# Kernel tuning notes

Measured on AMD Instinct MI355X. Metric: run time of the kernel, lower is better.

The kernel has to match this reference:

```python
import jax, jax.numpy as jnp
import numpy as np

B, N, C = 8, 512, 256
HID_E = 32          # edge_pred hidden width
FILTERS = (64, 64, 64)
OUT = 2


def setup_inputs() -> dict:
    key = jax.random.key(0)
    ks = jax.random.split(key, 12)
    s = 0.05
    inp = {
        "x": jax.random.normal(ks[0], (B, N, C), jnp.float32),
        "A": jax.random.uniform(ks[1], (B, N, N), jnp.float32),
        "mask": jnp.ones((B, N), jnp.float32),
        # edge predictor: Linear(2C,32) -> ReLU -> Linear(32,1)
        "ew1": jax.random.normal(ks[2], (2 * C, HID_E), jnp.float32) * s,
        "eb1": jnp.zeros((HID_E,), jnp.float32),
        "ew2": jax.random.normal(ks[3], (HID_E, 1), jnp.float32) * s,
        "eb2": jnp.zeros((1,), jnp.float32),
        # GraphConv stack: Linear(in*n_relations, f) per layer (n_relations=2)
        "gw0": jax.random.normal(ks[4], (2 * C, FILTERS[0]), jnp.float32) * s,
        "gb0": jnp.zeros((FILTERS[0],), jnp.float32),
        "gw1": jax.random.normal(ks[5], (2 * FILTERS[0], FILTERS[1]), jnp.float32) * s,
        "gb1": jnp.zeros((FILTERS[1],), jnp.float32),
        "gw2": jax.random.normal(ks[6], (2 * FILTERS[1], FILTERS[2]), jnp.float32) * s,
        "gb2": jnp.zeros((FILTERS[2],), jnp.float32),
        # final classifier (dropout is identity in eval)
        "fcw": jax.random.normal(ks[7], (FILTERS[2], OUT), jnp.float32) * s,
        "fcb": jnp.zeros((OUT,), jnp.float32),
    }
    return inp


def _laplacian(A):
    # A_hat = A + I ; L = D^-1/2 A_hat D^-1/2 with D from row-sums (dim 1)
    n = A.shape[-1]
    A_hat = A + jnp.eye(n, dtype=A.dtype)
    D = (A_hat.sum(axis=1) + 1e-5) ** -0.5  # [B,N]
    return D[:, :, None] * A_hat * D[:, None, :]


def reference(x, A, mask, ew1, eb1, ew2, eb2, gw0, gb0, gw1, gb1, gw2, gb2, fcw, fcb):
    b, n, c = x.shape
    # edge MLP over all node pairs; first layer split so we never build [B,N,N,2C]
    wa, wb = ew1[:c], ew1[c:]
    xa = x @ wa  # [B,N,32] contribution of node i
    xb = x @ wb  # [B,N,32] contribution of node j
    h = jax.nn.relu(xa[:, :, None, :] + xb[:, None, :, :] + eb1)  # [B,N,N,32]
    e = (h @ ew2)[..., 0] + eb2[0]  # e[b,i,j] = edge_pred([x_i, x_j])
    # symmetrized score: exp(0.5 * (f(i,j) + f(j,i)))
    y = jnp.exp(0.5 * (e + jnp.swapaxes(e, 1, 2)))
    triu = jnp.triu(jnp.ones((n, n), bool), 1)
    valid = (mask[:, :, None] > 0) & (mask[:, None, :] > 0)
    A_pred = jnp.where(triu[None] & valid, y, 0.0)
    A_pred = A_pred + jnp.swapaxes(A_pred, 1, 2)

    # multi-relation GCN stack (relations: input A, predicted A_pred)
    L0 = _laplacian(A)
    L1 = _laplacian(A_pred)
    m = mask[:, :, None]
    h0 = x
    for W, bias in ((gw0, gb0), (gw1, gb1), (gw2, gb2)):
        xh = jnp.concatenate([L0 @ h0, L1 @ h0], axis=-1)  # [B,N,2*f_in]
        h0 = jax.nn.relu((xh @ W + bias) * m)
    g = h0.max(axis=1)  # [B, filters[-1]] global max pool over nodes
    return g @ fcw + fcb  # [B, OUT]
```

## Files before the change

kernel.cpp:

```cpp
#include <hip/hip_runtime.h>
#include <hip/hip_bf16.h>
#include <math.h>

#define NB 8
#define NN 512
#define NC 256
#define HID 32

typedef __attribute__((ext_vector_type(8))) short short8;
typedef __attribute__((ext_vector_type(4))) float float4v;
typedef unsigned short ushort_t;

__device__ __forceinline__ ushort_t f2bf(float x) {
    unsigned u = __float_as_uint(x);
    return (ushort_t)((u + 0x7fffu + ((u >> 16) & 1u)) >> 16);
}
__device__ __forceinline__ float bf2f(ushort_t h) {
    return __uint_as_float(((unsigned)h) << 16);
}

__global__ __launch_bounds__(256) void xaxb_gemm(
    const float* __restrict__ x, const float* __restrict__ ew1,
    const float* __restrict__ eb1, float* __restrict__ xab,
    float* __restrict__ dsum)
{
    __shared__ float sX[32][17];
    __shared__ float sW[32][68];
    int t = threadIdx.x;
    if (blockIdx.x < 32) dsum[blockIdx.x * 256 + t] = 0.f;
    int r0 = blockIdx.x * 16;
    int tx = t & 15, ty = t >> 4;
    float acc[4] = {0.f, 0.f, 0.f, 0.f};
    for (int k0 = 0; k0 < NC; k0 += 32) {
        {
            int kk = (t & 15) * 2, r = t >> 4;
            float2 v = *(const float2*)(x + (size_t)(r0 + r) * NC + k0 + kk);
            sX[kk][r] = v.x; sX[kk + 1][r] = v.y;
        }
        {
            int c4 = (t & 15) * 4;
            int half = c4 >> 5, cc = c4 & 31;
#pragma unroll
            for (int rr = 0; rr < 2; ++rr) {
                int kk = (t >> 4) + rr * 16;
                *(float4*)&sW[kk][c4] =
                    *(const float4*)(ew1 + (size_t)(half * NC + k0 + kk) * HID + cc);
            }
        }
        __syncthreads();
#pragma unroll
        for (int k = 0; k < 32; ++k) {
            float a = sX[k][ty];
            float4 w = *(const float4*)&sW[k][tx * 4];
            acc[0] = fmaf(a, w.x, acc[0]); acc[1] = fmaf(a, w.y, acc[1]);
            acc[2] = fmaf(a, w.z, acc[2]); acc[3] = fmaf(a, w.w, acc[3]);
        }
        __syncthreads();
    }
    int c4 = tx * 4;
    float4 o; o.x = acc[0]; o.y = acc[1]; o.z = acc[2]; o.w = acc[3];
    if (c4 >= 32) {
        o.x += eb1[c4 - 32]; o.y += eb1[c4 - 31];
        o.z += eb1[c4 - 30]; o.w += eb1[c4 - 29];
    }
    *(float4*)&xab[(size_t)(r0 + ty) * 64 + c4] = o;
}

__global__ __launch_bounds__(256) void edge_scores(
    const float* __restrict__ xab, const float* __restrict__ ew2,
    const float* __restrict__ eb2, const float* __restrict__ mask,
    const float* __restrict__ A, ushort_t* __restrict__ Ah,
    ushort_t* __restrict__ APh, float* __restrict__ dsum)
{
    __shared__ float sI[32][65], sJ[32][65];
    __shared__ float sV[32][33];
    __shared__ float w2[32];
    int b = blockIdx.z;
    int p = blockIdx.x;
    int X = 0;
    while ((X + 1) * 16 - ((X + 1) * X) / 2 <= p) ++X;
    int Y = X + (p - (X * 16 - (X * (X - 1)) / 2));
    int i0 = X * 32, j0 = Y * 32;
    int t = threadIdx.x;
    if (t < 32) w2[t] = ew2[t];
    {
        int c4 = (t & 15) * 4;
#pragma unroll
        for (int rr = 0; rr < 2; ++rr) {
            int r = (t >> 4) + rr * 16;
            float4 vi = *(const float4*)(xab + ((size_t)(b * NN + i0 + r)) * 64 + c4);
            float4 vj = *(const float4*)(xab + ((size_t)(b * NN + j0 + r)) * 64 + c4);
            sI[r][c4] = vi.x; sI[r][c4 + 1] = vi.y; sI[r][c4 + 2] = vi.z; sI[r][c4 + 3] = vi.w;
            sJ[r][c4] = vj.x; sJ[r][c4 + 1] = vj.y; sJ[r][c4 + 2] = vj.z; sJ[r][c4 + 3] = vj.w;
        }
    }
    __syncthreads();
    float eb2v = eb2[0];
#pragma unroll
    for (int pz = 0; pz < 4; ++pz) {
        int e = t + pz * 256;
        int ti = e >> 5, tj = e & 31;
        int i = i0 + ti, j = j0 + tj;
        float sij = 0.f, sji = 0.f;
#pragma unroll
        for (int k = 0; k < 32; ++k) {
            sij = fmaf(fmaxf(sI[ti][k] + sJ[tj][32 + k], 0.f), w2[k], sij);
            sji = fmaf(fmaxf(sJ[tj][k] + sI[ti][32 + k], 0.f), w2[k], sji);
        }
        bool ok = (i != j) && (mask[b * NN + i] > 0.f) && (mask[b * NN + j] > 0.f);
        sV[ti][tj] = ok ? expf(0.5f * (sij + sji) + eb2v) : 0.f;
    }
    __syncthreads();
#pragma unroll
    for (int pz = 0; pz < 4; ++pz) {
        int r = (t >> 5) + pz * 8, c = t & 31;
        size_t o1 = ((size_t)(b * NN + i0 + r)) * NN + j0 + c;
        size_t o2 = ((size_t)(b * NN + j0 + r)) * NN + i0 + c;
        APh[o1] = f2bf(sV[r][c]);
        APh[o2] = f2bf(sV[c][r]);
    }
    if (t < 32) {
        float s = 0.f;
#pragma unroll
        for (int r = 0; r < 32; ++r) s += sV[r][t];
        atomicAdd(&dsum[(NB * NN) + b * NN + j0 + t], s);
    } else if (t < 64 && X != Y) {
        int c = t - 32;
        float s = 0.f;
#pragma unroll
        for (int j = 0; j < 32; ++j) s += sV[c][j];
        atomicAdd(&dsum[(NB * NN) + b * NN + i0 + c], s);
    }
    if (p < 128) {
        const float* Ar = A + ((size_t)b * NN + 4 * p) * NN;
        ushort_t* Hr = Ah + ((size_t)b * NN + 4 * p) * NN;
        float s0 = 0.f, s1 = 0.f;
#pragma unroll
        for (int rr = 0; rr < 4; ++rr) {
            float a0 = Ar[(size_t)rr * NN + t];
            float a1 = Ar[(size_t)rr * NN + t + 256];
            Hr[(size_t)rr * NN + t] = f2bf(a0);
            Hr[(size_t)rr * NN + t + 256] = f2bf(a1);
            s0 += a0; s1 += a1;
        }
        atomicAdd(&dsum[b * NN + t], s0);
        atomicAdd(&dsum[b * NN + t + 256], s1);
    }
}

__global__ __launch_bounds__(256) void pre_gemmT(
    const float* __restrict__ h, const float* __restrict__ gw,
    const float* __restrict__ dsum, ushort_t* __restrict__ PTh, int Cin)
{
    __shared__ float sH[32][17];
    __shared__ float sW[32][132];
    __shared__ __align__(16) ushort_t sTh[128][24];
    int r0 = blockIdx.x * 16;
    int t = threadIdx.x;
    int tx = t & 31, ty = t >> 5;
    float acc0[4] = {0.f, 0.f, 0.f, 0.f};
    float acc1[4] = {0.f, 0.f, 0.f, 0.f};
    for (int k0 = 0; k0 < Cin; k0 += 32) {
        {
            int kk = (t & 15) * 2, r = t >> 4;
            float2 v = *(const float2*)(h + (size_t)(r0 + r) * Cin + k0 + kk);
            sH[kk][r] = v.x; sH[kk + 1][r] = v.y;
        }
        {
            int c4 = (t & 31) * 4;
            int half = c4 >> 6, cc = c4 & 63;
#pragma unroll
            for (int rr = 0; rr < 4; ++rr) {
                int kk = (t >> 5) + rr * 8;
                *(float4*)&sW[kk][c4] =
                    *(const float4*)(gw + (size_t)(half * Cin + k0 + kk) * 64 + cc);
            }
        }
        __syncthreads();
#pragma unroll
        for (int k = 0; k < 32; ++k) {
            float a0 = sH[k][ty * 2];
            float a1 = sH[k][ty * 2 + 1];
            float4 w = *(const float4*)&sW[k][tx * 4];
            acc0[0] = fmaf(a0, w.x, acc0[0]); acc0[1] = fmaf(a0, w.y, acc0[1]);
            acc0[2] = fmaf(a0, w.z, acc0[2]); acc0[3] = fmaf(a0, w.w, acc0[3]);
            acc1[0] = fmaf(a1, w.x, acc1[0]); acc1[1] = fmaf(a1, w.y, acc1[1]);
            acc1[2] = fmaf(a1, w.z, acc1[2]); acc1[3] = fmaf(a1, w.w, acc1[3]);
        }
        __syncthreads();
    }
    int c4 = tx * 4;
    const float* draw = dsum + ((c4 >= 64) ? (NB * NN) : 0);
#pragma unroll
    for (int r = 0; r < 2; ++r) {
        int rl = ty * 2 + r;
        int row = r0 + rl;
        float d = rsqrtf(draw[row] + 1.0f + 1e-5f);
        float* ap = (r == 0) ? acc0 : acc1;
#pragma unroll
        for (int n = 0; n < 4; ++n)
            sTh[c4 + n][rl] = f2bf(d * ap[n]);
    }
    __syncthreads();
    {
        int c = t & 127, half = t >> 7;
        int bb = r0 >> 9, ibase = r0 & (NN - 1);
        ushort_t* dst = PTh + ((size_t)(bb * 128 + c)) * NN + ibase + half * 8;
        *(short8*)dst = *(const short8*)&sTh[c][half * 8];
    }
}

__global__ __launch_bounds__(256) void fused_mfma(
    const ushort_t* __restrict__ Ah, const ushort_t* __restrict__ APh,
    const ushort_t* __restrict__ PTh, const float* __restrict__ dsum,
    const float* __restrict__ bias, const float* __restrict__ mask,
    float* __restrict__ Hout)
{
    __shared__ __align__(16) ushort_t sA[2][16][72];
    __shared__ __align__(16) ushort_t sPh[64][72];
    __shared__ float sRed[2][32][17];
    int b = blockIdx.z, ch = blockIdx.y, i0 = blockIdx.x * 16;
    int t = threadIdx.x;
    int lane = t & 63, w = t >> 6;
    int quad = lane >> 4, m16 = lane & 15;
    int lap = w >> 1;
    float4v acc = {0.f, 0.f, 0.f, 0.f};

    int sa_arr = t >> 7, sa_id = t & 127;
    int sa_r = sa_id >> 3, sa_q = sa_id & 7;
    const ushort_t* sa_src = (sa_arr ? APh : Ah)
        + ((size_t)(b * NN + i0 + sa_r)) * NN + sa_q * 8;

    for (int k0 = 0; k0 < NN; k0 += 64) {
        __syncthreads();
        *(short8*)&sA[sa_arr][sa_r][sa_q * 8] = *(const short8*)(sa_src + k0);
#pragma unroll
        for (int cc = 0; cc < 2; ++cc) {
            int chunk = t + cc * 256;
            int l = chunk >> 3, q = chunk & 7;
            int colg = (l >> 5) * 64 + ch * 32 + (l & 31);
            const ushort_t* src = PTh + ((size_t)(b * 128 + colg)) * NN + k0 + q * 8;
            *(short8*)&sPh[l][q * 8] = *(const short8*)src;
        }
        __syncthreads();
#pragma unroll
        for (int kh = 0; kh < 2; ++kh) {
            int ko = kh * 32 + quad * 8;
            short8 ph = *(const short8*)&sPh[w * 16 + m16][ko];
            short8 av = *(const short8*)&sA[lap][m16][ko];
            acc = __builtin_amdgcn_mfma_f32_16x16x32_bf16(ph, av, acc, 0, 0, 0);
        }
    }
    int gi = b * NN + i0 + m16;
    float d = rsqrtf(dsum[lap * (NB * NN) + gi] + 1.0f + 1e-5f);
    int cbase = (w & 1) * 16 + quad * 4;
#pragma unroll
    for (int r = 0; r < 4; ++r) {
        int c32 = cbase + r;
        int pcol = lap * 64 + ch * 32 + c32;
        size_t pidx = ((size_t)(b * 128 + pcol)) * NN + i0 + m16;
        float pv = bf2f(PTh[pidx]);
        sRed[lap][c32][m16] = d * (acc[r] + pv);
    }
    __syncthreads();
#pragma unroll
    for (int s = 0; s < 2; ++s) {
        int idx = t + s * 256;
        int c32 = idx & 31, i = idx >> 5;
        int gi2 = b * NN + i0 + i;
        float v = (sRed[0][c32][i] + sRed[1][c32][i] + bias[ch * 32 + c32]) * mask[gi2];
        Hout[(size_t)gi2 * 64 + ch * 32 + c32] = fmaxf(v, 0.f);
    }
}

__global__ __launch_bounds__(256) void final_fc(
    const float* __restrict__ H, const float* __restrict__ fcw,
    const float* __restrict__ fcb, float* __restrict__ out)
{
    __shared__ float red[4][64];
    __shared__ float g[64];
    int b = blockIdx.x;
    int o = threadIdx.x & 63, seg = threadIdx.x >> 6;
    const float* Hb = H + (size_t)b * NN * 64;
    float mx = -INFINITY;
    for (int i = seg; i < NN; i += 4) mx = fmaxf(mx, Hb[(size_t)i * 64 + o]);
    red[seg][o] = mx;
    __syncthreads();
    if (seg == 0)
        g[o] = fmaxf(fmaxf(red[0][o], red[1][o]), fmaxf(red[2][o], red[3][o]));
    __syncthreads();
    if (threadIdx.x < 2) {
        float acc = fcb[threadIdx.x];
        for (int k = 0; k < 64; ++k) acc = fmaf(g[k], fcw[k * 2 + threadIdx.x], acc);
        out[b * 2 + threadIdx.x] = acc;
    }
}

extern "C" void kernel_launch(void* const* d_in, const int* in_sizes, int n_in,
                              void* d_out, int out_size, void* d_ws, size_t ws_size,
                              hipStream_t stream)
{
    const float* x    = (const float*)d_in[0];
    const float* A    = (const float*)d_in[1];
    const float* mask = (const float*)d_in[2];
    const float* ew1  = (const float*)d_in[3];
    const float* eb1  = (const float*)d_in[4];
    const float* ew2  = (const float*)d_in[5];
    const float* eb2  = (const float*)d_in[6];
    const float* gw0  = (const float*)d_in[7];
    const float* gb0  = (const float*)d_in[8];
    const float* gw1  = (const float*)d_in[9];
    const float* gb1  = (const float*)d_in[10];
    const float* gw2  = (const float*)d_in[11];
    const float* gb2  = (const float*)d_in[12];
    const float* fcw  = (const float*)d_in[13];
    const float* fcb  = (const float*)d_in[14];
    float* out = (float*)d_out;
    char* ws = (char*)d_ws;

    const size_t NEL = (size_t)NB * NN * NN;
    float*    xab  = (float*)ws;                       ws += 262144 * 4;
    ushort_t* APh  = (ushort_t*)ws;                    ws += NEL * 2;
    ushort_t* Ahs  = (ushort_t*)ws;                    ws += NEL * 2;
    float*    dsum = (float*)ws;                       ws += 8192 * 4;
    ushort_t* PTh  = (ushort_t*)ws;                    ws += 524288 * 2;
    float*    hA   = (float*)ws;                       ws += 262144 * 4;
    float*    hB   = (float*)ws;                       ws += 262144 * 4;

    xaxb_gemm  <<<256, 256, 0, stream>>>(x, ew1, eb1, xab, dsum);
    edge_scores<<<dim3(136, 1, NB), 256, 0, stream>>>(xab, ew2, eb2, mask,
                                                      A, Ahs, APh, dsum);

    pre_gemmT <<<256, 256, 0, stream>>>(x, gw0, dsum, PTh, 256);
    fused_mfma<<<dim3(32, 2, NB), 256, 0, stream>>>(Ahs, APh, PTh,
                                                    dsum, gb0, mask, hA);
    pre_gemmT <<<256, 256, 0, stream>>>(hA, gw1, dsum, PTh, 64);
    fused_mfma<<<dim3(32, 2, NB), 256, 0, stream>>>(Ahs, APh, PTh,
                                                    dsum, gb1, mask, hB);
    pre_gemmT <<<256, 256, 0, stream>>>(hB, gw2, dsum, PTh, 64);
    fused_mfma<<<dim3(32, 2, NB), 256, 0, stream>>>(Ahs, APh, PTh,
                                                    dsum, gb2, mask, hA);

    final_fc<<<NB, 256, 0, stream>>>(hA, fcw, fcb, out);
}
```

Measured before the change: 182.6 us.

## Fuse all stages into one persistent kernel with grid-wide atomic barriers

Replaces the nine separate kernel launches with a single persistent kernel of 256 blocks. The blocks move through the edge-score, GCN pre-GEMM, MFMA aggregation and final-FC phases, separated by software grid barriers built on an atomic counter. Shared memory is overlaid through a union. This removes launch gaps and inter-kernel drain, but adds barrier spin cost and relies on all 256 blocks being co-resident. Work per phase is also rebalanced over a fixed grid, so phases with 1088 tiles now loop.

```diff
diff --git a/kernel.cpp b/kernel.cpp
--- a/kernel.cpp
+++ b/kernel.cpp
@@ -6,6 +6,7 @@
 #define NN 512
 #define NC 256
 #define HID 32
+#define GD 256
 
 typedef __attribute__((ext_vector_type(8))) short short8;
 typedef __attribute__((ext_vector_type(4))) float float4v;
@@ -19,280 +20,305 @@
     return __uint_as_float(((unsigned)h) << 16);
 }
 
-__global__ __launch_bounds__(256) void xaxb_gemm(
-    const float* __restrict__ x, const float* __restrict__ ew1,
-    const float* __restrict__ eb1, float* __restrict__ xab,
-    float* __restrict__ dsum)
+__device__ __forceinline__ void gbar(int* cnt, int target) {
+    __syncthreads();
+    if (threadIdx.x == 0) {
+        __threadfence();
+        atomicAdd(cnt, 1);
+        while (__hip_atomic_load(cnt, __ATOMIC_RELAXED,
+                                 __HIP_MEMORY_SCOPE_AGENT) < target)
+            __builtin_amdgcn_s_sleep(2);
+        __threadfence();
+    }
+    __syncthreads();
+}
+
+struct Params {
+    const float *x, *A, *mask, *ew1, *eb1, *ew2, *eb2;
+    const float *gw0, *gb0, *gw1, *gb1, *gw2, *gb2, *fcw, *fcb;
+    float* out;
+    int*   bar;
+    float* xab;
+    ushort_t* APh;
+    ushort_t* Ahs;
+    float* dsum;
+    ushort_t* PTh;
+    float* hA;
+    float* hB;
+};
+
+union SharedT {
+    struct { float sX[32][17]; float sW[32][68]; } p1;
+    struct { float sI[32][65]; float sJ[32][65]; float sV[32][33]; float w2[32]; } p2;
+    struct { float sH[32][17]; float sW[32][132]; ushort_t sTh[128][24]; } p3;
+    struct { ushort_t sA[2][16][72]; ushort_t sPh[64][72]; float sRed[2][32][17]; } p4;
+    struct { float red[4][64]; float g[64]; } p5;
+};
+
+__global__ void bar_init(int* bar) { if (threadIdx.x < 64) bar[threadIdx.x] = 0; }
+
+__global__ __launch_bounds__(256, 1) void mega(Params P)
 {
-    __shared__ float sX[32][17];
-    __shared__ float sW[32][68];
+    __shared__ __align__(16) SharedT sh;
     int t = threadIdx.x;
-    if (blockIdx.x < 32) dsum[blockIdx.x * 256 + t] = 0.f;
-    int r0 = blockIdx.x * 16;
-    int tx = t & 15, ty = t >> 4;
-    float acc[4] = {0.f, 0.f, 0.f, 0.f};
-    for (int k0 = 0; k0 < NC; k0 += 32) {
-        {
-            int kk = (t & 15) * 2, r = t >> 4;
-            float2 v = *(const float2*)(x + (size_t)(r0 + r) * NC + k0 + kk);
-            sX[kk][r] = v.x; sX[kk + 1][r] = v.y;
-        }
+    int bid = blockIdx.x;
+    int barn = 0;
+
+    if (bid < 32) P.dsum[bid * 256 + t] = 0.f;
+    for (int r0 = bid * 16; r0 < 4096 * 0 + (bid + 1) * 16; r0 += 16) {
+        int tx = t & 15, ty = t >> 4;
+        float acc[4] = {0.f, 0.f, 0.f, 0.f};
+        for (int k0 = 0; k0 < NC; k0 += 32) {
+            {
+                int kk = (t & 15) * 2, r = t >> 4;
+                float2 v = *(const float2*)(P.x + (size_t)(r0 + r) * NC + k0 + kk);
+                sh.p1.sX[kk][r] = v.x; sh.p1.sX[kk + 1][r] = v.y;
+            }
+            {
+                int c4 = (t & 15) * 4;
+                int half = c4 >> 5, cc = c4 & 31;
+#pragma unroll
+                for (int rr = 0; rr < 2; ++rr) {
+                    int kk = (t >> 4) + rr * 16;
+                    *(float4*)&sh.p1.sW[kk][c4] =
+                        *(const float4*)(P.ew1 + (size_t)(half * NC + k0 + kk) * HID + cc);
+                }
+            }
+            __syncthreads();
+#pragma unroll
+            for (int k = 0; k < 32; ++k) {
+                float a = sh.p1.sX[k][ty];
+                float4 w = *(const float4*)&sh.p1.sW[k][tx * 4];
+                acc[0] = fmaf(a, w.x, acc[0]); acc[1] = fmaf(a, w.y, acc[1]);
+                acc[2] = fmaf(a, w.z, acc[2]); acc[3] = fmaf(a, w.w, acc[3]);
+            }
+            __syncthreads();
+        }
+        int c4 = tx * 4;
+        float4 o; o.x = acc[0]; o.y = acc[1]; o.z = acc[2]; o.w = acc[3];
+        if (c4 >= 32) {
+            o.x += P.eb1[c4 - 32]; o.y += P.eb1[c4 - 31];
+            o.z += P.eb1[c4 - 30]; o.w += P.eb1[c4 - 29];
+        }
+        *(float4*)&P.xab[(size_t)(r0 + ty) * 64 + c4] = o;
+    }
+    gbar(P.bar, ++barn * GD);
+
+    for (int u = bid; u < 136 * NB; u += GD) {
+        __syncthreads();
+        int b = u / 136, p = u - b * 136;
+        int X = 0;
+        while ((X + 1) * 16 - ((X + 1) * X) / 2 <= p) ++X;
+        int Y = X + (p - (X * 16 - (X * (X - 1)) / 2));
+        int i0 = X * 32, j0 = Y * 32;
+        if (t < 32) sh.p2.w2[t] = P.ew2[t];
         {
             int c4 = (t & 15) * 4;
-            int half = c4 >> 5, cc = c4 & 31;
 #pragma unroll
             for (int rr = 0; rr < 2; ++rr) {
-                int kk = (t >> 4) + rr * 16;
-                *(float4*)&sW[kk][c4] =
-                    *(const float4*)(ew1 + (size_t)(half * NC + k0 + kk) * HID + cc);
-            }
-        }
-        __syncthreads();
-#pragma unroll
-        for (int k = 0; k < 32; ++k) {
-            float a = sX[k][ty];
-            float4 w = *(const float4*)&sW[k][tx * 4];
-            acc[0] = fmaf(a, w.x, acc[0]); acc[1] = fmaf(a, w.y, acc[1]);
-            acc[2] = fmaf(a, w.z, acc[2]); acc[3] = fmaf(a, w.w, acc[3]);
-        }
-        __syncthreads();
-    }
-    int c4 = tx * 4;
-    float4 o; o.x = acc[0]; o.y = acc[1]; o.z = acc[2]; o.w = acc[3];
-    if (c4 >= 32) {
-        o.x += eb1[c4 - 32]; o.y += eb1[c4 - 31];
-        o.z += eb1[c4 - 30]; o.w += eb1[c4 - 29];
-    }
-    *(float4*)&xab[(size_t)(r0 + ty) * 64 + c4] = o;
-}
-
-__global__ __launch_bounds__(256) void edge_scores(
-    const float* __restrict__ xab, const float* __restrict__ ew2,
-    const float* __restrict__ eb2, const float* __restrict__ mask,
-    const float* __restrict__ A, ushort_t* __restrict__ Ah,
-    ushort_t* __restrict__ APh, float* __restrict__ dsum)
-{
-    __shared__ float sI[32][65], sJ[32][65];
-    __shared__ float sV[32][33];
-    __shared__ float w2[32];
-    int b = blockIdx.z;
-    int p = blockIdx.x;
-    int X = 0;
-    while ((X + 1) * 16 - ((X + 1) * X) / 2 <= p) ++X;
-    int Y = X + (p - (X * 16 - (X * (X - 1)) / 2));
-    int i0 = X * 32, j0 = Y * 32;
-    int t = threadIdx.x;
-    if (t < 32) w2[t] = ew2[t];
-    {
-        int c4 = (t & 15) * 4;
-#pragma unroll
-        for (int rr = 0; rr < 2; ++rr) {
-            int r = (t >> 4) + rr * 16;
-            float4 vi = *(const float4*)(xab + ((size_t)(b * NN + i0 + r)) * 64 + c4);
-            float4 vj = *(const float4*)(xab + ((size_t)(b * NN + j0 + r)) * 64 + c4);
-            sI[r][c4] = vi.x; sI[r][c4 + 1] = vi.y; sI[r][c4 + 2] = vi.z; sI[r][c4 + 3] = vi.w;
-            sJ[r][c4] = vj.x; sJ[r][c4 + 1] = vj.y; sJ[r][c4 + 2] = vj.z; sJ[r][c4 + 3] = vj.w;
-        }
-    }
-    __syncthreads();
-    float eb2v = eb2[0];
-#pragma unroll
-    for (int pz = 0; pz < 4; ++pz) {
-        int e = t + pz * 256;
-        int ti = e >> 5, tj = e & 31;
-        int i = i0 + ti, j = j0 + tj;
-        float sij = 0.f, sji = 0.f;
-#pragma unroll
-        for (int k = 0; k < 32; ++k) {
-            sij = fmaf(fmaxf(sI[ti][k] + sJ[tj][32 + k], 0.f), w2[k], sij);
-            sji = fmaf(fmaxf(sJ[tj][k] + sI[ti][32 + k], 0.f), w2[k], sji);
-        }
-        bool ok = (i != j) && (mask[b * NN + i] > 0.f) && (mask[b * NN + j] > 0.f);
-        sV[ti][tj] = ok ? expf(0.5f * (sij + sji) + eb2v) : 0.f;
-    }
-    __syncthreads();
-#pragma unroll
-    for (int pz = 0; pz < 4; ++pz) {
-        int r = (t >> 5) + pz * 8, c = t & 31;
-        size_t o1 = ((size_t)(b * NN + i0 + r)) * NN + j0 + c;
-        size_t o2 = ((size_t)(b * NN + j0 + r)) * NN + i0 + c;
-        APh[o1] = f2bf(sV[r][c]);
-        APh[o2] = f2bf(sV[c][r]);
-    }
-    if (t < 32) {
-        float s = 0.f;
-#pragma unroll
-        for (int r = 0; r < 32; ++r) s += sV[r][t];
-        atomicAdd(&dsum[(NB * NN) + b * NN + j0 + t], s);
-    } else if (t < 64 && X != Y) {
-        int c = t - 32;
-        float s = 0.f;
-#pragma unroll
-        for (int j = 0; j < 32; ++j) s += sV[c][j];
-        atomicAdd(&dsum[(NB * NN) + b * NN + i0 + c], s);
-    }
-    if (p < 128) {
-        const float* Ar = A + ((size_t)b * NN + 4 * p) * NN;
-        ushort_t* Hr = Ah + ((size_t)b * NN + 4 * p) * NN;
-        float s0 = 0.f, s1 = 0.f;
-#pragma unroll
-        for (int rr = 0; rr < 4; ++rr) {
-            float a0 = Ar[(size_t)rr * NN + t];
-            float a1 = Ar[(size_t)rr * NN + t + 256];
-            Hr[(size_t)rr * NN + t] = f2bf(a0);
-            Hr[(size_t)rr * NN + t + 256] = f2bf(a1);
-            s0 += a0; s1 += a1;
-        }
-        atomicAdd(&dsum[b * NN + t], s0);
-        atomicAdd(&dsum[b * NN + t + 256], s1);
-    }
-}
-
-__global__ __launch_bounds__(256) void pre_gemmT(
-    const float* __restrict__ h, const float* __restrict__ gw,
-    const float* __restrict__ dsum, ushort_t* __restrict__ PTh, int Cin)
-{
-    __shared__ float sH[32][17];
-    __shared__ float sW[32][132];
-    __shared__ __align__(16) ushort_t sTh[128][24];
-    int r0 = blockIdx.x * 16;
-    int t = threadIdx.x;
-    int tx = t & 31, ty = t >> 5;
-    float acc0[4] = {0.f, 0.f, 0.f, 0.f};
-    float acc1[4] = {0.f, 0.f, 0.f, 0.f};
-    for (int k0 = 0; k0 < Cin; k0 += 32) {
-        {
-            int kk = (t & 15) * 2, r = t >> 4;
-            float2 v = *(const float2*)(h + (size_t)(r0 + r) * Cin + k0 + kk);
-            sH[kk][r] = v.x; sH[kk + 1][r] = v.y;
-        }
-        {
-            int c4 = (t & 31) * 4;
-            int half = c4 >> 6, cc = c4 & 63;
+                int r = (t >> 4) + rr * 16;
+                float4 vi = *(const float4*)(P.xab + ((size_t)(b * NN + i0 + r)) * 64 + c4);
+                float4 vj = *(const float4*)(P.xab + ((size_t)(b * NN + j0 + r)) * 64 + c4);
+                sh.p2.sI[r][c4] = vi.x; sh.p2.sI[r][c4 + 1] = vi.y;
+                sh.p2.sI[r][c4 + 2] = vi.z; sh.p2.sI[r][c4 + 3] = vi.w;
+                sh.p2.sJ[r][c4] = vj.x; sh.p2.sJ[r][c4 + 1] = vj.y;
+                sh.p2.sJ[r][c4 + 2] = vj.z; sh.p2.sJ[r][c4 + 3] = vj.w;
+            }
+        }
+        __syncthreads();
+        float eb2v = P.eb2[0];
+#pragma unroll
+        for (int pz = 0; pz < 4; ++pz) {
+            int e = t + pz * 256;
+            int ti = e >> 5, tj = e & 31;
+            int i = i0 + ti, j = j0 + tj;
+            float sij = 0.f, sji = 0.f;
+#pragma unroll
+            for (int k = 0; k < 32; ++k) {
+                sij = fmaf(fmaxf(sh.p2.sI[ti][k] + sh.p2.sJ[tj][32 + k], 0.f), sh.p2.w2[k], sij);
+                sji = fmaf(fmaxf(sh.p2.sJ[tj][k] + sh.p2.sI[ti][32 + k], 0.f), sh.p2.w2[k], sji);
+            }
+            bool ok = (i != j) && (P.mask[b * NN + i] > 0.f) && (P.mask[b * NN + j] > 0.f);
+            sh.p2.sV[ti][tj] = ok ? expf(0.5f * (sij + sji) + eb2v) : 0.f;
+        }
+        __syncthreads();
+#pragma unroll
+        for (int pz = 0; pz < 4; ++pz) {
+            int r = (t >> 5) + pz * 8, c = t & 31;
+            size_t o1 = ((size_t)(b * NN + i0 + r)) * NN + j0 + c;
+            size_t o2 = ((size_t)(b * NN + j0 + r)) * NN + i0 + c;
+            P.APh[o1] = f2bf(sh.p2.sV[r][c]);
+            P.APh[o2] = f2bf(sh.p2.sV[c][r]);
+        }
+        if (t < 32) {
+            float s = 0.f;
+#pragma unroll
+            for (int r = 0; r < 32; ++r) s += sh.p2.sV[r][t];
+            atomicAdd(&P.dsum[(NB * NN) + b * NN + j0 + t], s);
+        } else if (t < 64 && X != Y) {
+            int c = t - 32;
+            float s = 0.f;
+#pragma unroll
+            for (int j = 0; j < 32; ++j) s += sh.p2.sV[c][j];
+            atomicAdd(&P.dsum[(NB * NN) + b * NN + i0 + c], s);
+        }
+        if (p < 128) {
+            const float* Ar = P.A + ((size_t)b * NN + 4 * p) * NN;
+            ushort_t* Hr = P.Ahs + ((size_t)b * NN + 4 * p) * NN;
+            float s0 = 0.f, s1 = 0.f;
 #pragma unroll
             for (int rr = 0; rr < 4; ++rr) {
-                int kk = (t >> 5) + rr * 8;
-                *(float4*)&sW[kk][c4] =
-                    *(const float4*)(gw + (size_t)(half * Cin + k0 + kk) * 64 + cc);
-            }
-        }
-        __syncthreads();
-#pragma unroll
-        for (int k = 0; k < 32; ++k) {
-            float a0 = sH[k][ty * 2];
-            float a1 = sH[k][ty * 2 + 1];
-            float4 w = *(const float4*)&sW[k][tx * 4];
-            acc0[0] = fmaf(a0, w.x, acc0[0]); acc0[1] = fmaf(a0, w.y, acc0[1]);
-            acc0[2] = fmaf(a0, w.z, acc0[2]); acc0[3] = fmaf(a0, w.w, acc0[3]);
-            acc1[0] = fmaf(a1, w.x, acc1[0]); acc1[1] = fmaf(a1, w.y, acc1[1]);
-            acc1[2] = fmaf(a1, w.z, acc1[2]); acc1[3] = fmaf(a1, w.w, acc1[3]);
-        }
-        __syncthreads();
-    }
-    int c4 = tx * 4;
-    const float* draw = dsum + ((c4 >= 64) ? (NB * NN) : 0);
-#pragma unroll
-    for (int r = 0; r < 2; ++r) {
-        int rl = ty * 2 + r;
-        int row = r0 + rl;
-        float d = rsqrtf(draw[row] + 1.0f + 1e-5f);
-        float* ap = (r == 0) ? acc0 : acc1;
-#pragma unroll
-        for (int n = 0; n < 4; ++n)
-            sTh[c4 + n][rl] = f2bf(d * ap[n]);
-    }
-    __syncthreads();
-    {
-        int c = t & 127, half = t >> 7;
-        int bb = r0 >> 9, ibase = r0 & (NN - 1);
-        ushort_t* dst = PTh + ((size_t)(bb * 128 + c)) * NN + ibase + half * 8;
-        *(short8*)dst = *(const short8*)&sTh[c][half * 8];
-    }
-}
-
-__global__ __launch_bounds__(256) void fused_mfma(
-    const ushort_t* __restrict__ Ah, const ushort_t* __restrict__ APh,
-    const ushort_t* __restrict__ PTh, const float* __restrict__ dsum,
-    const float* __restrict__ bias, const float* __restrict__ mask,
-    float* __restrict__ Hout)
-{
-    __shared__ __align__(16) ushort_t sA[2][16][72];
-    __shared__ __align__(16) ushort_t sPh[64][72];
-    __shared__ float sRed[2][32][17];
-    int b = blockIdx.z, ch = blockIdx.y, i0 = blockIdx.x * 16;
-    int t = threadIdx.x;
+                float a0 = Ar[(size_t)rr * NN + t];
+                float a1 = Ar[(size_t)rr * NN + t + 256];
+                Hr[(size_t)rr * NN + t] = f2bf(a0);
+                Hr[(size_t)rr * NN + t + 256] = f2bf(a1);
+                s0 += a0; s1 += a1;
+            }
+            atomicAdd(&P.dsum[b * NN + t], s0);
+            atomicAdd(&P.dsum[b * NN + t + 256], s1);
+        }
+    }
+    gbar(P.bar, ++barn * GD);
+
     int lane = t & 63, w = t >> 6;
     int quad = lane >> 4, m16 = lane & 15;
     int lap = w >> 1;
-    float4v acc = {0.f, 0.f, 0.f, 0.f};
-
     int sa_arr = t >> 7, sa_id = t & 127;
     int sa_r = sa_id >> 3, sa_q = sa_id & 7;
-    const ushort_t* sa_src = (sa_arr ? APh : Ah)
-        + ((size_t)(b * NN + i0 + sa_r)) * NN + sa_q * 8;
-
-    for (int k0 = 0; k0 < NN; k0 += 64) {
-        __syncthreads();
-        *(short8*)&sA[sa_arr][sa_r][sa_q * 8] = *(const short8*)(sa_src + k0);
-#pragma unroll
-        for (int cc = 0; cc < 2; ++cc) {
-            int chunk = t + cc * 256;
-            int l = chunk >> 3, q = chunk & 7;
-            int colg = (l >> 5) * 64 + ch * 32 + (l & 31);
-            const ushort_t* src = PTh + ((size_t)(b * 128 + colg)) * NN + k0 + q * 8;
-            *(short8*)&sPh[l][q * 8] = *(const short8*)src;
-        }
-        __syncthreads();
-#pragma unroll
-        for (int kh = 0; kh < 2; ++kh) {
-            int ko = kh * 32 + quad * 8;
-            short8 ph = *(const short8*)&sPh[w * 16 + m16][ko];
-            short8 av = *(const short8*)&sA[lap][m16][ko];
-            acc = __builtin_amdgcn_mfma_f32_16x16x32_bf16(ph, av, acc, 0, 0, 0);
-        }
-    }
-    int gi = b * NN + i0 + m16;
-    float d = rsqrtf(dsum[lap * (NB * NN) + gi] + 1.0f + 1e-5f);
-    int cbase = (w & 1) * 16 + quad * 4;
-#pragma unroll
-    for (int r = 0; r < 4; ++r) {
-        int c32 = cbase + r;
-        int pcol = lap * 64 + ch * 32 + c32;
-        size_t pidx = ((size_t)(b * 128 + pcol)) * NN + i0 + m16;
-        float pv = bf2f(PTh[pidx]);
-        sRed[lap][c32][m16] = d * (acc[r] + pv);
-    }
-    __syncthreads();
-#pragma unroll
-    for (int s = 0; s < 2; ++s) {
-        int idx = t + s * 256;
-        int c32 = idx & 31, i = idx >> 5;
-        int gi2 = b * NN + i0 + i;
-        float v = (sRed[0][c32][i] + sRed[1][c32][i] + bias[ch * 32 + c32]) * mask[gi2];
-        Hout[(size_t)gi2 * 64 + ch * 32 + c32] = fmaxf(v, 0.f);
-    }
-}
-
-__global__ __launch_bounds__(256) void final_fc(
-    const float* __restrict__ H, const float* __restrict__ fcw,
-    const float* __restrict__ fcb, float* __restrict__ out)
-{
-    __shared__ float red[4][64];
-    __shared__ float g[64];
-    int b = blockIdx.x;
-    int o = threadIdx.x & 63, seg = threadIdx.x >> 6;
-    const float* Hb = H + (size_t)b * NN * 64;
-    float mx = -INFINITY;
-    for (int i = seg; i < NN; i += 4) mx = fmaxf(mx, Hb[(size_t)i * 64 + o]);
-    red[seg][o] = mx;
-    __syncthreads();
-    if (seg == 0)
-        g[o] = fmaxf(fmaxf(red[0][o], red[1][o]), fmaxf(red[2][o], red[3][o]));
-    __syncthreads();
-    if (threadIdx.x < 2) {
-        float acc = fcb[threadIdx.x];
-        for (int k = 0; k < 64; ++k) acc = fmaf(g[k], fcw[k * 2 + threadIdx.x], acc);
-        out[b * 2 + threadIdx.x] = acc;
+
+    for (int L = 0; L < 3; ++L) {
+        const float* hsrc = (L == 0) ? P.x : ((L == 1) ? P.hA : P.hB);
+        const float* gw   = (L == 0) ? P.gw0 : ((L == 1) ? P.gw1 : P.gw2);
+        const float* gb   = (L == 0) ? P.gb0 : ((L == 1) ? P.gb1 : P.gb2);
+        float* hout       = (L == 1) ? P.hB : P.hA;
+        int Cin           = (L == 0) ? NC : 64;
+
+        {
+            int r0 = bid * 16;
+            int tx = t & 31, ty = t >> 5;
+            float acc0[4] = {0.f, 0.f, 0.f, 0.f};
+            float acc1[4] = {0.f, 0.f, 0.f, 0.f};
+            for (int k0 = 0; k0 < Cin; k0 += 32) {
+                __syncthreads();
+                {
+                    int kk = (t & 15) * 2, r = t >> 4;
+                    float2 v = *(const float2*)(hsrc + (size_t)(r0 + r) * Cin + k0 + kk);
+                    sh.p3.sH[kk][r] = v.x; sh.p3.sH[kk + 1][r] = v.y;
+                }
+                {
+                    int c4 = (t & 31) * 4;
+                    int half = c4 >> 6, cc = c4 & 63;
+#pragma unroll
+                    for (int rr = 0; rr < 4; ++rr) {
+                        int kk = (t >> 5) + rr * 8;
+                        *(float4*)&sh.p3.sW[kk][c4] =
+                            *(const float4*)(gw + (size_t)(half * Cin + k0 + kk) * 64 + cc);
+                    }
+                }
+                __syncthreads();
+#pragma unroll
+                for (int k = 0; k < 32; ++k) {
+                    float a0 = sh.p3.sH[k][ty * 2];
+                    float a1 = sh.p3.sH[k][ty * 2 + 1];
+                    float4 ww = *(const float4*)&sh.p3.sW[k][tx * 4];
+                    acc0[0] = fmaf(a0, ww.x, acc0[0]); acc0[1] = fmaf(a0, ww.y, acc0[1]);
+                    acc0[2] = fmaf(a0, ww.z, acc0[2]); acc0[3] = fmaf(a0, ww.w, acc0[3]);
+                    acc1[0] = fmaf(a1, ww.x, acc1[0]); acc1[1] = fmaf(a1, ww.y, acc1[1]);
+                    acc1[2] = fmaf(a1, ww.z, acc1[2]); acc1[3] = fmaf(a1, ww.w, acc1[3]);
+                }
+            }
+            __syncthreads();
+            int c4 = tx * 4;
+            const float* draw = P.dsum + ((c4 >= 64) ? (NB * NN) : 0);
+#pragma unroll
+            for (int r = 0; r < 2; ++r) {
+                int rl = ty * 2 + r;
+                int row = r0 + rl;
+                float d = rsqrtf(draw[row] + 1.0f + 1e-5f);
+                float* ap = (r == 0) ? acc0 : acc1;
+#pragma unroll
+                for (int n = 0; n < 4; ++n)
+                    sh.p3.sTh[c4 + n][rl] = f2bf(d * ap[n]);
+            }
+            __syncthreads();
+            {
+                int c = t & 127, half = t >> 7;
+                int bb = r0 >> 9, ibase = r0 & (NN - 1);
+                ushort_t* dst = P.PTh + ((size_t)(bb * 128 + c)) * NN + ibase + half * 8;
+                *(short8*)dst = *(const short8*)&sh.p3.sTh[c][half * 8];
+            }
+        }
+        gbar(P.bar, ++barn * GD);
+
+        for (int fu = bid; fu < 512; fu += GD) {
+            int fb = fu >> 6, frem = fu & 63;
+            int fch = frem >> 5, fi0 = (frem & 31) * 16;
+            const ushort_t* sa_src = (sa_arr ? P.APh : P.Ahs)
+                + ((size_t)(fb * NN + fi0 + sa_r)) * NN + sa_q * 8;
+            float4v acc = {0.f, 0.f, 0.f, 0.f};
+            for (int k0 = 0; k0 < NN; k0 += 64) {
+                __syncthreads();
+                *(short8*)&sh.p4.sA[sa_arr][sa_r][sa_q * 8] = *(const short8*)(sa_src + k0);
+#pragma unroll
+                for (int cc = 0; cc < 2; ++cc) {
+                    int chunk = t + cc * 256;
+                    int l = chunk >> 3, q = chunk & 7;
+                    int colg = (l >> 5) * 64 + fch * 32 + (l & 31);
+                    const ushort_t* src = P.PTh + ((size_t)(fb * 128 + colg)) * NN + k0 + q * 8;
+                    *(short8*)&sh.p4.sPh[l][q * 8] = *(const short8*)src;
+                }
+                __syncthreads();
+#pragma unroll
+                for (int kh = 0; kh < 2; ++kh) {
+                    int ko = kh * 32 + quad * 8;
+                    short8 ph = *(const short8*)&sh.p4.sPh[w * 16 + m16][ko];
+                    short8 av = *(const short8*)&sh.p4.sA[lap][m16][ko];
+                    acc = __builtin_amdgcn_mfma_f32_16x16x32_bf16(ph, av, acc, 0, 0, 0);
+                }
+            }
+            int gi = fb * NN + fi0 + m16;
+            float d = rsqrtf(P.dsum[lap * (NB * NN) + gi] + 1.0f + 1e-5f);
+            int cbase = (w & 1) * 16 + quad * 4;
+            __syncthreads();
+#pragma unroll
+            for (int r = 0; r < 4; ++r) {
+                int c32 = cbase + r;
+                int pcol = lap * 64 + fch * 32 + c32;
+                size_t pidx = ((size_t)(fb * 128 + pcol)) * NN + fi0 + m16;
+                float pv = bf2f(P.PTh[pidx]);
+                sh.p4.sRed[lap][c32][m16] = d * (acc[r] + pv);
+            }
+            __syncthreads();
+#pragma unroll
+            for (int s = 0; s < 2; ++s) {
+                int idx = t + s * 256;
+                int c32 = idx & 31, i = idx >> 5;
+                int gi2 = fb * NN + fi0 + i;
+                float v = (sh.p4.sRed[0][c32][i] + sh.p4.sRed[1][c32][i]
+                           + gb[fch * 32 + c32]) * P.mask[gi2];
+                hout[(size_t)gi2 * 64 + fch * 32 + c32] = fmaxf(v, 0.f);
+            }
+        }
+        gbar(P.bar, ++barn * GD);
+    }
+
+    if (bid < NB) {
+        int b = bid;
+        int o = t & 63, seg = t >> 6;
+        const float* Hb = P.hA + (size_t)b * NN * 64;
+        float mx = -INFINITY;
+        for (int i = seg; i < NN; i += 4) mx = fmaxf(mx, Hb[(size_t)i * 64 + o]);
+        sh.p5.red[seg][o] = mx;
+        __syncthreads();
+        if (seg == 0)
+            sh.p5.g[o] = fmaxf(fmaxf(sh.p5.red[0][o], sh.p5.red[1][o]),
+                               fmaxf(sh.p5.red[2][o], sh.p5.red[3][o]));
+        __syncthreads();
+        if (t < 2) {
+            float acc = P.fcb[t];
+            for (int k = 0; k < 64; ++k) acc = fmaf(sh.p5.g[k], P.fcw[k * 2 + t], acc);
+            P.out[b * 2 + t] = acc;
+        }
     }
 }
 
@@ -300,46 +326,36 @@
                               void* d_out, int out_size, void* d_ws, size_t ws_size,
                               hipStream_t stream)
 {
-    const float* x    = (const float*)d_in[0];
-    const float* A    = (const float*)d_in[1];
-    const float* mask = (const float*)d_in[2];
-    const float* ew1  = (const float*)d_in[3];
-    const float* eb1  = (const float*)d_in[4];
-    const float* ew2  = (const float*)d_in[5];
-    const float* eb2  = (const float*)d_in[6];
-    const float* gw0  = (const float*)d_in[7];
-    const float* gb0  = (const float*)d_in[8];
-    const float* gw1  = (const float*)d_in[9];
-    const float* gb1  = (const float*)d_in[10];
-    const float* gw2  = (const float*)d_in[11];
-    const float* gb2  = (const float*)d_in[12];
-    const float* fcw  = (const float*)d_in[13];
-    const float* fcb  = (const float*)d_in[14];
-    float* out = (float*)d_out;
     char* ws = (char*)d_ws;
-
     const size_t NEL = (size_t)NB * NN * NN;
-    float*    xab  = (float*)ws;                       ws += 262144 * 4;
-    ushort_t* APh  = (ushort_t*)ws;                    ws += NEL * 2;
-    ushort_t* Ahs  = (ushort_t*)ws;                    ws += NEL * 2;
-    float*    dsum = (float*)ws;                       ws += 8192 * 4;
-    ushort_t* PTh  = (ushort_t*)ws;                    ws += 524288 * 2;
-    float*    hA   = (float*)ws;                       ws += 262144 * 4;
-    float*    hB   = (float*)ws;                       ws += 262144 * 4;
-
-    xaxb_gemm  <<<256, 256, 0, stream>>>(x, ew1, eb1, xab, dsum);
-    edge_scores<<<dim3(136, 1, NB), 256, 0, stream>>>(xab, ew2, eb2, mask,
-                                                      A, Ahs, APh, dsum);
-
-    pre_gemmT <<<256, 256, 0, stream>>>(x, gw0, dsum, PTh, 256);
-    fused_mfma<<<dim3(32, 2, NB), 256, 0, stream>>>(Ahs, APh, PTh,
-                                                    dsum, gb0, mask, hA);
-    pre_gemmT <<<256, 256, 0, stream>>>(hA, gw1, dsum, PTh, 64);
-    fused_mfma<<<dim3(32, 2, NB), 256, 0, stream>>>(Ahs, APh, PTh,
-                                                    dsum, gb1, mask, hB);
-    pre_gemmT <<<256, 256, 0, stream>>>(hB, gw2, dsum, PTh, 64);
-    fused_mfma<<<dim3(32, 2, NB), 256, 0, stream>>>(Ahs, APh, PTh,
-                                                    dsum, gb2, mask, hA);
-
-    final_fc<<<NB, 256, 0, stream>>>(hA, fcw, fcb, out);
-}
+
+    Params P;
+    P.x    = (const float*)d_in[0];
+    P.A    = (const float*)d_in[1];
+    P.mask = (const float*)d_in[2];
+    P.ew1  = (const float*)d_in[3];
+    P.eb1  = (const float*)d_in[4];
+    P.ew2  = (const float*)d_in[5];
+    P.eb2  = (const float*)d_in[6];
+    P.gw0  = (const float*)d_in[7];
+    P.gb0  = (const float*)d_in[8];
+    P.gw1  = (const float*)d_in[9];
+    P.gb1  = (const float*)d_in[10];
+    P.gw2  = (const float*)d_in[11];
+    P.gb2  = (const float*)d_in[12];
+    P.fcw  = (const float*)d_in[13];
+    P.fcb  = (const float*)d_in[14];
+    P.out  = (float*)d_out;
+
+    P.bar  = (int*)ws;                      ws += 64 * 4;
+    P.xab  = (float*)ws;                    ws += 262144 * 4;
+    P.APh  = (ushort_t*)ws;                 ws += NEL * 2;
+    P.Ahs  = (ushort_t*)ws;                 ws += NEL * 2;
+    P.dsum = (float*)ws;                    ws += 8192 * 4;
+    P.PTh  = (ushort_t*)ws;                 ws += 524288 * 2;
+    P.hA   = (float*)ws;                    ws += 262144 * 4;
+    P.hB   = (float*)ws;                    ws += 262144 * 4;
+
+    bar_init<<<1, 64, 0, stream>>>(P.bar);
+    mega<<<GD, 256, 0, stream>>>(P);
+}
```

After: 369.7 us. +102.4%, slower.

## Fuse next-layer projection and final max-pool/FC into each GCN aggregation kernel

Applied to the files above, without the earlier changes.

Merges the Laplacian aggregation kernel with the following layer's weight projection (pre_gemmT) and, for the last layer, with the global max-pool and classifier via atomicMax plus a last-block counter. Each block now covers all 64 output channels for 16 rows, so the channel-split grid shrinks from 512 to 256 blocks, and the intermediate fp32 H round trips through global memory go away. This removes three kernel launches and the H writes and reads. In exchange each block carries more shared memory and serial work, the grid is smaller, and the unsigned-bit atomicMax only orders correctly because post-ReLU values are non-negative.

```diff
diff --git a/kernel.cpp b/kernel.cpp
--- a/kernel.cpp
+++ b/kernel.cpp
@@ -22,12 +22,16 @@
 __global__ __launch_bounds__(256) void xaxb_gemm(
     const float* __restrict__ x, const float* __restrict__ ew1,
     const float* __restrict__ eb1, float* __restrict__ xab,
-    float* __restrict__ dsum)
+    float* __restrict__ dsum, unsigned* __restrict__ gmax, int* __restrict__ done)
 {
     __shared__ float sX[32][17];
     __shared__ float sW[32][68];
     int t = threadIdx.x;
     if (blockIdx.x < 32) dsum[blockIdx.x * 256 + t] = 0.f;
+    if (blockIdx.x == 32) {
+        gmax[t] = 0u; gmax[t + 256] = 0u;
+        if (t < NB) done[t] = 0;
+    }
     int r0 = blockIdx.x * 16;
     int tx = t & 15, ty = t >> 4;
     float acc[4] = {0.f, 0.f, 0.f, 0.f};
@@ -210,89 +214,160 @@
     }
 }
 
-__global__ __launch_bounds__(256) void fused_mfma(
+__global__ __launch_bounds__(256) void fused_layer(
     const ushort_t* __restrict__ Ah, const ushort_t* __restrict__ APh,
-    const ushort_t* __restrict__ PTh, const float* __restrict__ dsum,
-    const float* __restrict__ bias, const float* __restrict__ mask,
-    float* __restrict__ Hout)
+    const ushort_t* __restrict__ PTin, ushort_t* __restrict__ PTout,
+    const float* __restrict__ dsum, const float* __restrict__ gb,
+    const float* __restrict__ mask, const float* __restrict__ gwN,
+    unsigned* __restrict__ gmax, int* __restrict__ done,
+    const float* __restrict__ fcw, const float* __restrict__ fcb,
+    float* __restrict__ out, int mode)
 {
-    __shared__ __align__(16) ushort_t sA[2][16][72];
-    __shared__ __align__(16) ushort_t sPh[64][72];
-    __shared__ float sRed[2][32][17];
-    int b = blockIdx.z, ch = blockIdx.y, i0 = blockIdx.x * 16;
+    __shared__ union {
+        struct { ushort_t sA[2][16][72]; ushort_t sPh[128][72]; } f;
+        struct { float sW[32][132]; ushort_t sTh[128][24]; } p;
+    } u;
+    __shared__ float sRed[2][64][17];
+    __shared__ float sH16[16][68];
+    __shared__ int   lastFlag;
+
     int t = threadIdx.x;
+    int fb = blockIdx.x >> 5;
+    int fi0 = (blockIdx.x & 31) * 16;
     int lane = t & 63, w = t >> 6;
     int quad = lane >> 4, m16 = lane & 15;
-    int lap = w >> 1;
-    float4v acc = {0.f, 0.f, 0.f, 0.f};
+    int lap = w >> 1, cg = w & 1;
 
     int sa_arr = t >> 7, sa_id = t & 127;
     int sa_r = sa_id >> 3, sa_q = sa_id & 7;
     const ushort_t* sa_src = (sa_arr ? APh : Ah)
-        + ((size_t)(b * NN + i0 + sa_r)) * NN + sa_q * 8;
+        + ((size_t)(fb * NN + fi0 + sa_r)) * NN + sa_q * 8;
+    float4v acc0 = {0.f, 0.f, 0.f, 0.f};
+    float4v acc1 = {0.f, 0.f, 0.f, 0.f};
 
     for (int k0 = 0; k0 < NN; k0 += 64) {
         __syncthreads();
-        *(short8*)&sA[sa_arr][sa_r][sa_q * 8] = *(const short8*)(sa_src + k0);
-#pragma unroll
-        for (int cc = 0; cc < 2; ++cc) {
+        *(short8*)&u.f.sA[sa_arr][sa_r][sa_q * 8] = *(const short8*)(sa_src + k0);
+#pragma unroll
+        for (int cc = 0; cc < 4; ++cc) {
             int chunk = t + cc * 256;
             int l = chunk >> 3, q = chunk & 7;
-            int colg = (l >> 5) * 64 + ch * 32 + (l & 31);
-            const ushort_t* src = PTh + ((size_t)(b * 128 + colg)) * NN + k0 + q * 8;
-            *(short8*)&sPh[l][q * 8] = *(const short8*)src;
+            const ushort_t* src = PTin + ((size_t)(fb * 128 + l)) * NN + k0 + q * 8;
+            *(short8*)&u.f.sPh[l][q * 8] = *(const short8*)src;
         }
         __syncthreads();
 #pragma unroll
         for (int kh = 0; kh < 2; ++kh) {
             int ko = kh * 32 + quad * 8;
-            short8 ph = *(const short8*)&sPh[w * 16 + m16][ko];
-            short8 av = *(const short8*)&sA[lap][m16][ko];
-            acc = __builtin_amdgcn_mfma_f32_16x16x32_bf16(ph, av, acc, 0, 0, 0);
-        }
-    }
-    int gi = b * NN + i0 + m16;
+            short8 av = *(const short8*)&u.f.sA[lap][m16][ko];
+            short8 p0 = *(const short8*)&u.f.sPh[lap * 64 + cg * 16 + m16][ko];
+            short8 p1 = *(const short8*)&u.f.sPh[lap * 64 + 32 + cg * 16 + m16][ko];
+            acc0 = __builtin_amdgcn_mfma_f32_16x16x32_bf16(p0, av, acc0, 0, 0, 0);
+            acc1 = __builtin_amdgcn_mfma_f32_16x16x32_bf16(p1, av, acc1, 0, 0, 0);
+        }
+    }
+    int gi = fb * NN + fi0 + m16;
     float d = rsqrtf(dsum[lap * (NB * NN) + gi] + 1.0f + 1e-5f);
-    int cbase = (w & 1) * 16 + quad * 4;
-#pragma unroll
-    for (int r = 0; r < 4; ++r) {
-        int c32 = cbase + r;
-        int pcol = lap * 64 + ch * 32 + c32;
-        size_t pidx = ((size_t)(b * 128 + pcol)) * NN + i0 + m16;
-        float pv = bf2f(PTh[pidx]);
-        sRed[lap][c32][m16] = d * (acc[r] + pv);
-    }
-    __syncthreads();
-#pragma unroll
-    for (int s = 0; s < 2; ++s) {
+    int cbase = cg * 16 + quad * 4;
+    __syncthreads();
+#pragma unroll
+    for (int ch = 0; ch < 2; ++ch) {
+        const float4v* ap = ch ? &acc1 : &acc0;
+#pragma unroll
+        for (int r = 0; r < 4; ++r) {
+            int c64 = ch * 32 + cbase + r;
+            size_t pidx = ((size_t)(fb * 128 + lap * 64 + c64)) * NN + fi0 + m16;
+            sRed[lap][c64][m16] = d * ((*ap)[r] + bf2f(PTin[pidx]));
+        }
+    }
+    __syncthreads();
+#pragma unroll
+    for (int s = 0; s < 4; ++s) {
         int idx = t + s * 256;
-        int c32 = idx & 31, i = idx >> 5;
-        int gi2 = b * NN + i0 + i;
-        float v = (sRed[0][c32][i] + sRed[1][c32][i] + bias[ch * 32 + c32]) * mask[gi2];
-        Hout[(size_t)gi2 * 64 + ch * 32 + c32] = fmaxf(v, 0.f);
-    }
-}
-
-__global__ __launch_bounds__(256) void final_fc(
-    const float* __restrict__ H, const float* __restrict__ fcw,
-    const float* __restrict__ fcb, float* __restrict__ out)
-{
-    __shared__ float red[4][64];
-    __shared__ float g[64];
-    int b = blockIdx.x;
-    int o = threadIdx.x & 63, seg = threadIdx.x >> 6;
-    const float* Hb = H + (size_t)b * NN * 64;
-    float mx = -INFINITY;
-    for (int i = seg; i < NN; i += 4) mx = fmaxf(mx, Hb[(size_t)i * 64 + o]);
-    red[seg][o] = mx;
-    __syncthreads();
-    if (seg == 0)
-        g[o] = fmaxf(fmaxf(red[0][o], red[1][o]), fmaxf(red[2][o], red[3][o]));
-    __syncthreads();
-    if (threadIdx.x < 2) {
-        float acc = fcb[threadIdx.x];
-        for (int k = 0; k < 64; ++k) acc = fmaf(g[k], fcw[k * 2 + threadIdx.x], acc);
-        out[b * 2 + threadIdx.x] = acc;
+        int c = idx & 63, r = idx >> 6;
+        float mv = mask[fb * NN + fi0 + r];
+        float v = (sRed[0][c][r] + sRed[1][c][r] + gb[c]) * mv;
+        sH16[r][c] = fmaxf(v, 0.f);
+    }
+    __syncthreads();
+
+    if (mode == 0) {
+        int tx = t & 31, ty = t >> 5;
+        float b0[4] = {0.f, 0.f, 0.f, 0.f};
+        float b1[4] = {0.f, 0.f, 0.f, 0.f};
+        for (int k0 = 0; k0 < 64; k0 += 32) {
+            __syncthreads();
+            {
+                int c4 = (t & 31) * 4;
+                int half = c4 >> 6, cc = c4 & 63;
+#pragma unroll
+                for (int rr = 0; rr < 4; ++rr) {
+                    int kk = (t >> 5) + rr * 8;
+                    *(float4*)&u.p.sW[kk][c4] =
+                        *(const float4*)(gwN + (size_t)(half * 64 + k0 + kk) * 64 + cc);
+                }
+            }
+            __syncthreads();
+#pragma unroll
+            for (int k = 0; k < 32; ++k) {
+                float a0 = sH16[ty * 2][k0 + k];
+                float a1 = sH16[ty * 2 + 1][k0 + k];
+                float4 ww = *(const float4*)&u.p.sW[k][tx * 4];
+                b0[0] = fmaf(a0, ww.x, b0[0]); b0[1] = fmaf(a0, ww.y, b0[1]);
+                b0[2] = fmaf(a0, ww.z, b0[2]); b0[3] = fmaf(a0, ww.w, b0[3]);
+                b1[0] = fmaf(a1, ww.x, b1[0]); b1[1] = fmaf(a1, ww.y, b1[1]);
+                b1[2] = fmaf(a1, ww.z, b1[2]); b1[3] = fmaf(a1, ww.w, b1[3]);
+            }
+        }
+        __syncthreads();
+        int c4 = tx * 4;
+        const float* draw = dsum + ((c4 >= 64) ? (NB * NN) : 0);
+#pragma unroll
+        for (int r = 0; r < 2; ++r) {
+            int rl = ty * 2 + r;
+            float dd = rsqrtf(draw[fb * NN + fi0 + rl] + 1.0f + 1e-5f);
+            float* ap = (r == 0) ? b0 : b1;
+#pragma unroll
+            for (int n = 0; n < 4; ++n)
+                u.p.sTh[c4 + n][rl] = f2bf(dd * ap[n]);
+        }
+        __syncthreads();
+        {
+            int c = t & 127, half = t >> 7;
+            ushort_t* dst = PTout + ((size_t)(fb * 128 + c)) * NN + fi0 + half * 8;
+            *(short8*)dst = *(const short8*)&u.p.sTh[c][half * 8];
+        }
+    } else {
+        if (t < 64) {
+            float mx = 0.f;
+#pragma unroll
+            for (int r = 0; r < 16; ++r) mx = fmaxf(mx, sH16[r][t]);
+            atomicMax(&gmax[fb * 64 + t], __float_as_uint(mx));
+        }
+        __syncthreads();
+        if (t == 0) {
+            __threadfence();
+            int old = atomicAdd(&done[fb], 1);
+            lastFlag = (old == 31);
+            __threadfence();
+        }
+        __syncthreads();
+        if (lastFlag) {
+            if (t < 64) {
+                unsigned ub = __hip_atomic_load(&gmax[fb * 64 + t],
+                                                __ATOMIC_RELAXED,
+                                                __HIP_MEMORY_SCOPE_AGENT);
+                sH16[0][t] = __uint_as_float(ub);
+            }
+            __syncthreads();
+            if (t < 2) {
+                float acc = fcb[t];
+#pragma unroll
+                for (int k = 0; k < 64; ++k)
+                    acc = fmaf(sH16[0][k], fcw[k * 2 + t], acc);
+                out[fb * 2 + t] = acc;
+            }
+        }
     }
 }
 
@@ -319,27 +394,24 @@
     char* ws = (char*)d_ws;
 
     const size_t NEL = (size_t)NB * NN * NN;
-    float*    xab  = (float*)ws;                       ws += 262144 * 4;
-    ushort_t* APh  = (ushort_t*)ws;                    ws += NEL * 2;
-    ushort_t* Ahs  = (ushort_t*)ws;                    ws += NEL * 2;
-    float*    dsum = (float*)ws;                       ws += 8192 * 4;
-    ushort_t* PTh  = (ushort_t*)ws;                    ws += 524288 * 2;
-    float*    hA   = (float*)ws;                       ws += 262144 * 4;
-    float*    hB   = (float*)ws;                       ws += 262144 * 4;
-
-    xaxb_gemm  <<<256, 256, 0, stream>>>(x, ew1, eb1, xab, dsum);
+    float*    xab  = (float*)ws;                   ws += 262144 * 4;
+    ushort_t* APh  = (ushort_t*)ws;                ws += NEL * 2;
+    ushort_t* Ahs  = (ushort_t*)ws;                ws += NEL * 2;
+    float*    dsum = (float*)ws;                   ws += 8192 * 4;
+    ushort_t* PT_A = (ushort_t*)ws;                ws += 524288 * 2;
+    ushort_t* PT_B = (ushort_t*)ws;                ws += 524288 * 2;
+    unsigned* gmax = (unsigned*)ws;                ws += 512 * 4;
+    int*      done = (int*)ws;                     ws += 64 * 4;
+
+    xaxb_gemm  <<<256, 256, 0, stream>>>(x, ew1, eb1, xab, dsum, gmax, done);
     edge_scores<<<dim3(136, 1, NB), 256, 0, stream>>>(xab, ew2, eb2, mask,
                                                       A, Ahs, APh, dsum);
-
-    pre_gemmT <<<256, 256, 0, stream>>>(x, gw0, dsum, PTh, 256);
-    fused_mfma<<<dim3(32, 2, NB), 256, 0, stream>>>(Ahs, APh, PTh,
-                                                    dsum, gb0, mask, hA);
-    pre_gemmT <<<256, 256, 0, stream>>>(hA, gw1, dsum, PTh, 64);
-    fused_mfma<<<dim3(32, 2, NB), 256, 0, stream>>>(Ahs, APh, PTh,
-                                                    dsum, gb1, mask, hB);
-    pre_gemmT <<<256, 256, 0, stream>>>(hB, gw2, dsum, PTh, 64);
-    fused_mfma<<<dim3(32, 2, NB), 256, 0, stream>>>(Ahs, APh, PTh,
-                                                    dsum, gb2, mask, hA);
-
-    final_fc<<<NB, 256, 0, stream>>>(hA, fcw, fcb, out);
-}
+    pre_gemmT  <<<256, 256, 0, stream>>>(x, gw0, dsum, PT_A, 256);
+
+    fused_layer<<<256, 256, 0, stream>>>(Ahs, APh, PT_A, PT_B, dsum, gb0, mask,
+                                         gw1, gmax, done, fcw, fcb, out, 0);
+    fused_layer<<<256, 256, 0, stream>>>(Ahs, APh, PT_B, PT_A, dsum, gb1, mask,
+                                         gw2, gmax, done, fcw, fcb, out, 0);
+    fused_layer<<<256, 256, 0, stream>>>(Ahs, APh, PT_A, PT_B, dsum, gb2, mask,
+                                         gw2, gmax, done, fcw, fcb, out, 1);
+}
```

New measurement: 197.3 us. 1.08x slower.
